# Kernel optimization log

Hardware: AMD Instinct MI355X
Metric: run time of the kernel (lower is better)

Reference implementation:

```python
import jax, jax.numpy as jnp
import numpy as np

D_MODEL = 1024
N_HEADS = 16
D_K = D_MODEL // N_HEADS


def setup_inputs() -> dict:
    key = jax.random.key(0)
    ks = jax.random.split(key, 12)
    B, S, D, H = 2, 2048, D_MODEL, N_HEADS
    s = 1.0 / np.sqrt(D)
    inp = {
        "x": jax.random.normal(ks[0], (B, S, D), jnp.float32),
        "Wq": jax.random.normal(ks[1], (D, D), jnp.float32) * s,
        "bq": jnp.zeros((D,), jnp.float32),
        "Wk": jax.random.normal(ks[2], (D, D), jnp.float32) * s,
        "bk": jnp.zeros((D,), jnp.float32),
        "Wv": jax.random.normal(ks[3], (D, D), jnp.float32) * s,
        "bv": jnp.zeros((D,), jnp.float32),
        "Wo": jax.random.normal(ks[4], (D, D), jnp.float32) * s,
        "bo": jnp.zeros((D,), jnp.float32),
        "Wp": jax.random.normal(ks[5], (D, H), jnp.float32) * s,
        "bp": jnp.zeros((H,), jnp.float32),
        "alpha": jax.random.normal(ks[6], (H,), jnp.float32) * 0.1,
    }
    return inp


def reference(x, Wq, bq, Wk, bk, Wv, bv, Wo, bo, Wp, bp, alpha):
    B, S, D = x.shape
    H, dk = N_HEADS, D_K
    scale = dk ** -0.5
    # projections -> (B, H, S, dk)
    Q = (x @ Wq + bq).reshape(B, S, H, dk).transpose(0, 2, 1, 3)
    K = (x @ Wk + bk).reshape(B, S, H, dk).transpose(0, 2, 1, 3)
    V = (x @ Wv + bv).reshape(B, S, H, dk).transpose(0, 2, 1, 3)
    scores = jnp.einsum("bhid,bhjd->bhij", Q, K) * scale  # (B,H,S,S)
    # phase derived from x: (B,S,H) -> (B,H,S)
    phase = (x @ Wp + bp).transpose(0, 2, 1)
    # coherence(i,j) = cos(phi_i - phi_j), per batch/head
    coherence = jnp.cos(phase[:, :, :, None] - phase[:, :, None, :])
    scores = scores + alpha[None, :, None, None] * coherence
    attn = jax.nn.softmax(scores, axis=-1)
    out = jnp.einsum("bhij,bhjd->bhid", attn, V)  # (B,H,S,dk)
    out = out.transpose(0, 2, 1, 3).reshape(B, S, D)
    return out @ Wo + bo
```

## Files before the change

### kernel.cpp

```cpp
#include <hip/hip_runtime.h>
#include <math.h>


#define S_LEN 2048
#define NHEADS 16

typedef __attribute__((ext_vector_type(8))) short short8;
typedef __attribute__((ext_vector_type(4))) float floatx4;
typedef __attribute__((ext_vector_type(4))) unsigned int uintx4;

__device__ inline unsigned short f2bf(float f) {
    union { float f; unsigned int i; } v; v.f = f;
    unsigned int u = v.i;
    return (unsigned short)((u + 0x7fffu + ((u >> 16) & 1u)) >> 16);
}
__device__ inline unsigned int pack2_bf16(float hi, float lo) {
    union { float f; unsigned int u; } a, b; a.f = hi; b.f = lo;
    return __builtin_amdgcn_perm(a.u, b.u, 0x07060302u);
}
__device__ inline void async_copy16(const unsigned short* src, unsigned short* dst_lds) {
    __builtin_amdgcn_global_load_lds(
        (const __attribute__((address_space(1))) unsigned int*)(src),
        (__attribute__((address_space(3))) unsigned int*)(dst_lds), 16, 0, 0);
}
__device__ inline void async_copy4(const float* src, float* dst_lds) {
    __builtin_amdgcn_global_load_lds(
        (const __attribute__((address_space(1))) unsigned int*)(src),
        (__attribute__((address_space(3))) unsigned int*)(dst_lds), 4, 0, 0);
}

__global__ __launch_bounds__(256) void prep_kernel(
    const float* __restrict__ x, const float* __restrict__ Wp,
    const float* __restrict__ bp,
    const float* __restrict__ w0, const float* __restrict__ w1,
    const float* __restrict__ w2, const float* __restrict__ w3,
    unsigned short* __restrict__ d0, unsigned short* __restrict__ d1,
    unsigned short* __restrict__ d2, unsigned short* __restrict__ d3,
    float* __restrict__ cosP, float* __restrict__ sinP,
    unsigned short* __restrict__ xb) {
    __shared__ __align__(16) unsigned short shmem[64 * 72];
    int t = threadIdx.x;
    if (blockIdx.x < 4096) {
        float* red = reinterpret_cast<float*>(shmem);
        int bid = blockIdx.x;
        int b = bid >> 11, s = bid & 2047;
        int h = t & 15, c = t >> 4;
        const float* xr = x + (size_t)bid * 1024;
        {
            float4 xv = *reinterpret_cast<const float4*>(&xr[t * 4]);
            uint2 o;
            o.x = (unsigned int)f2bf(xv.x) | ((unsigned int)f2bf(xv.y) << 16);
            o.y = (unsigned int)f2bf(xv.z) | ((unsigned int)f2bf(xv.w) << 16);
            *reinterpret_cast<uint2*>(&xb[(size_t)bid * 1024 + t * 4]) = o;
        }
        float acc = 0.f;
#pragma unroll 8
        for (int kk = 0; kk < 64; kk++) {
            int k = c * 64 + kk;
            acc += xr[k] * Wp[k * 16 + h];
        }
        red[t] = acc;
        __syncthreads();
        if (t < 16) {
            float sum = 0.f;
#pragma unroll
            for (int c2 = 0; c2 < 16; c2++) sum += red[c2 * 16 + t];
            sum += bp[t];
            float sv, cv;
            __sincosf(sum, &sv, &cv);
            size_t o = ((size_t)b * NHEADS + t) * S_LEN + s;
            cosP[o] = cv; sinP[o] = sv;
        }
    } else {
        unsigned short (*tile)[72] = reinterpret_cast<unsigned short (*)[72]>(shmem);
        int bid = blockIdx.x - 4096;
        int mat = bid >> 8;
        int tl  = bid & 255;
        int tr = tl >> 4, tc = tl & 15;
        const float* src    = (mat == 0) ? w0 : (mat == 1) ? w1 : (mat == 2) ? w2 : w3;
        unsigned short* dst = (mat == 0) ? d0 : (mat == 1) ? d1 : (mat == 2) ? d2 : d3;
        int col = t & 63, rbase = (t >> 6) * 16;
#pragma unroll
        for (int i = 0; i < 16; i++) {
            int row = rbase + i;
            tile[row][col] = f2bf(src[(size_t)(tr * 64 + row) * 1024 + tc * 64 + col]);
        }
        __syncthreads();
#pragma unroll
        for (int i = 0; i < 16; i++) {
            int row = rbase + i;
            dst[(size_t)(tc * 64 + row) * 1024 + tr * 64 + col] = tile[col][row];
        }
    }
}

template <int MT>
__global__ __launch_bounds__(256) void gemm_bt(
    const unsigned short* __restrict__ A, const unsigned short* __restrict__ BT,
    int N, int mode,
    const float* __restrict__ b0, const float* __restrict__ b1,
    const float* __restrict__ b2,
    unsigned short* __restrict__ o0, unsigned short* __restrict__ o1,
    unsigned short* __restrict__ o2, float* __restrict__ of) {
    __shared__ __align__(16) unsigned short As[MT * 32];
    __shared__ __align__(16) unsigned short Bs[128 * 32];
    const int K = 1024;
    const int MI = MT / 32;
    int t = threadIdx.x;
    int mBase = blockIdx.x * MT;
    int nBase = blockIdx.y * 128;
    int w = t >> 6, lane = t & 63, l15 = lane & 15, quad = lane >> 4;
    int wm = (w & 1) * (MT / 2), wn = (w >> 1) * 64;
    floatx4 acc[MI][4];
#pragma unroll
    for (int i = 0; i < MI; i++)
#pragma unroll
        for (int j = 0; j < 4; j++) acc[i][j] = (floatx4){0.f, 0.f, 0.f, 0.f};

    int arow = t >> 2, aseg = (t & 3) * 8;
    for (int k0 = 0; k0 < K; k0 += 32) {
        __syncthreads();
#pragma unroll
        for (int i = 0; i < MT / 64; i++)
            async_copy16(&A[(size_t)(mBase + i * 64 + arow) * K + k0 + aseg],
                         &As[(i * 64 + arow) * 32 + aseg]);
#pragma unroll
        for (int i = 0; i < 2; i++)
            async_copy16(&BT[(size_t)(nBase + i * 64 + arow) * K + k0 + aseg],
                         &Bs[(i * 64 + arow) * 32 + aseg]);
        __syncthreads();
        short8 af[MI], bfr[4];
#pragma unroll
        for (int mi = 0; mi < MI; mi++)
            af[mi] = *reinterpret_cast<const short8*>(&As[(wm + mi * 16 + l15) * 32 + quad * 8]);
#pragma unroll
        for (int ni = 0; ni < 4; ni++)
            bfr[ni] = *reinterpret_cast<const short8*>(&Bs[(wn + ni * 16 + l15) * 32 + quad * 8]);
#pragma unroll
        for (int mi = 0; mi < MI; mi++)
#pragma unroll
            for (int ni = 0; ni < 4; ni++)
                acc[mi][ni] = __builtin_amdgcn_mfma_f32_16x16x32_bf16(af[mi], bfr[ni], acc[mi][ni], 0, 0, 0);
    }

#pragma unroll
    for (int mi = 0; mi < MI; mi++) {
        int rowB = mBase + wm + mi * 16 + quad * 4;
#pragma unroll
        for (int ni = 0; ni < 4; ni++) {
            int col = nBase + wn + ni * 16 + l15;
            if (mode == 0) {
                float bias = b0[col];
#pragma unroll
                for (int r = 0; r < 4; r++) {
                    of[(size_t)(rowB + r) * N + col] = acc[mi][ni][r] + bias;
                }
            } else {
                int mat = col >> 10, nn = col & 1023;
                int h = nn >> 6, d = nn & 63;
                int b = rowB >> 11, sidx = rowB & 2047;
                if (mat == 2) {
                    float bv = b2[nn];
                    int jj = sidx & 63;
                    int a2 = jj >> 5, c2 = (jj >> 4) & 1, bb = jj & 15;
                    size_t rowOff = ((size_t)((b * NHEADS + h) * 64 + d)) * S_LEN +
                                    (sidx & ~63) + a2 * 32 + c2;
#pragma unroll
                    for (int r = 0; r < 4; r++)
                        o2[rowOff + 2 * (bb + r)] = f2bf(acc[mi][ni][r] + bv);
                } else {
                    const float* bias  = (mat == 0) ? b0 : b1;
                    unsigned short* op = (mat == 0) ? o0 : o1;
                    float bv = bias[nn];
                    float scl = (mat == 0) ? 0.18033688f : 1.0f;
#pragma unroll
                    for (int r = 0; r < 4; r++) {
                        float cv = (acc[mi][ni][r] + bv) * scl;
                        op[(((size_t)b * NHEADS + h) * S_LEN + (sidx + r)) * 64 + d] = f2bf(cv);
                    }
                }
            }
        }
    }
}

__global__ __launch_bounds__(512) void attn_kernel(
    const unsigned short* __restrict__ Qg, const unsigned short* __restrict__ Kg,
    const unsigned short* __restrict__ VTg,
    const float* __restrict__ cosP, const float* __restrict__ sinP,
    const float* __restrict__ alpha, unsigned short* __restrict__ ctx) {
    __shared__ __align__(16) unsigned short KsB[2][64 * 64];
    __shared__ __align__(16) unsigned short VtB[2][64 * 64];
    __shared__ __align__(16) float csB[2][128];
    __shared__ __align__(16) unsigned short Plb[8][16 * 72];

    int bid = blockIdx.x;
    int bh = bid >> 4, qt = bid & 15;
    int t = threadIdx.x, w = t >> 6, lane = t & 63, l15 = lane & 15, quad = lane >> 4;
    int m0 = qt * 128 + w * 16;
    size_t base = (size_t)bh * (S_LEN * 64);
    size_t phBase = (size_t)bh * S_LEN;
    const float L2E = 1.44269504f;

    int sj = t >> 3, sg = t & 7;
    int srot = ((sg - (sj & 7)) & 7) * 8;

    short8 qf[2];
#pragma unroll
    for (int c = 0; c < 2; c++)
        qf[c] = *reinterpret_cast<const short8*>(
            &Qg[base + (size_t)(m0 + l15) * 64 + c * 32 + quad * 8]);

    float alph = alpha[bh & 15] * L2E;
    float ci[4], si[4];
#pragma unroll
    for (int r = 0; r < 4; r++) {
        size_t o = phBase + m0 + quad * 4 + r;
        ci[r] = alph * cosP[o];
        si[r] = alph * sinP[o];
    }

    {
        async_copy16(&Kg[base + (size_t)sj * 64 + srot], &KsB[0][t * 8]);
        async_copy16(&VTg[base + (size_t)sj * S_LEN + srot], &VtB[0][t * 8]);
        if (w == 2)      async_copy4(&cosP[phBase + lane], &csB[0][lane]);
        else if (w == 3) async_copy4(&sinP[phBase + lane], &csB[0][64 + lane]);
    }

    floatx4 oacc[4], lacc;
#pragma unroll
    for (int tt = 0; tt < 4; tt++) oacc[tt] = (floatx4){0.f, 0.f, 0.f, 0.f};
    lacc = (floatx4){0.f, 0.f, 0.f, 0.f};
    const short8 ones8 = {(short)0x3F80, (short)0x3F80, (short)0x3F80, (short)0x3F80,
                          (short)0x3F80, (short)0x3F80, (short)0x3F80, (short)0x3F80};

    int rot = l15 & 7;
    int cb0 = 16 * ((quad + rot) & 7);
    int cb1 = 16 * ((quad + 4 + rot) & 7);

    for (int kt = 0; kt < 32; kt++) {
        int p = kt & 1;
        __syncthreads();
        if (kt < 31) {
            int kn = kt + 1, pn = p ^ 1;
            async_copy16(&Kg[base + (size_t)(kn * 64 + sj) * 64 + srot], &KsB[pn][t * 8]);
            async_copy16(&VTg[base + (size_t)sj * S_LEN + kn * 64 + srot], &VtB[pn][t * 8]);
            if (w == 2)      async_copy4(&cosP[phBase + kn * 64 + lane], &csB[pn][lane]);
            else if (w == 3) async_copy4(&sinP[phBase + kn * 64 + lane], &csB[pn][64 + lane]);
        }

        floatx4 st[4];
#pragma unroll
        for (int jt = 0; jt < 4; jt++) {
            const char* kr = (const char*)&KsB[p][(jt * 16 + l15) * 64];
            short8 kf0 = *reinterpret_cast<const short8*>(kr + cb0);
            short8 kf1 = *reinterpret_cast<const short8*>(kr + cb1);
            floatx4 s = (floatx4){0.f, 0.f, 0.f, 0.f};
            s = __builtin_amdgcn_mfma_f32_16x16x32_bf16(qf[0], kf0, s, 0, 0, 0);
            s = __builtin_amdgcn_mfma_f32_16x16x32_bf16(qf[1], kf1, s, 0, 0, 0);
            st[jt] = s;
        }

        float cjv[4], sjv[4];
#pragma unroll
        for (int jt = 0; jt < 4; jt++) {
            cjv[jt] = csB[p][jt * 16 + l15];
            sjv[jt] = csB[p][64 + jt * 16 + l15];
        }

        unsigned int* pl = reinterpret_cast<unsigned int*>(&Plb[w][0]);
#pragma unroll
        for (int r = 0; r < 4; r++) {
            float cc = ci[r], ss = si[r];
            float p0 = __builtin_amdgcn_exp2f(st[0][r] + cc * cjv[0] + ss * sjv[0]);
            float p1 = __builtin_amdgcn_exp2f(st[1][r] + cc * cjv[1] + ss * sjv[1]);
            float p2 = __builtin_amdgcn_exp2f(st[2][r] + cc * cjv[2] + ss * sjv[2]);
            float p3 = __builtin_amdgcn_exp2f(st[3][r] + cc * cjv[3] + ss * sjv[3]);
            int row = quad * 4 + r;
            pl[row * 36 + l15]      = pack2_bf16(p1, p0);
            pl[row * 36 + 16 + l15] = pack2_bf16(p3, p2);
        }

        short8 pf[2];
#pragma unroll
        for (int c = 0; c < 2; c++)
            pf[c] = *reinterpret_cast<const short8*>(
                &Plb[w][l15 * 72 + c * 32 + quad * 8]);

#pragma unroll
        for (int c = 0; c < 2; c++) {
            int cb = c ? cb1 : cb0;
#pragma unroll
            for (int tt = 0; tt < 4; tt++) {
                const char* vr = (const char*)&VtB[p][(tt * 16 + l15) * 64];
                short8 vf = *reinterpret_cast<const short8*>(vr + cb);
                oacc[tt] = __builtin_amdgcn_mfma_f32_16x16x32_bf16(pf[c], vf, oacc[tt], 0, 0, 0);
            }
            lacc = __builtin_amdgcn_mfma_f32_16x16x32_bf16(pf[c], ones8, lacc, 0, 0, 0);
        }
    }

    int b = bh >> 4, h = bh & 15;
    float inv[4];
#pragma unroll
    for (int r = 0; r < 4; r++) inv[r] = 1.0f / lacc[r];
#pragma unroll
    for (int tt = 0; tt < 4; tt++)
#pragma unroll
        for (int r = 0; r < 4; r++) {
            int srow = m0 + quad * 4 + r;
            ctx[((size_t)(b * S_LEN + srow)) * 1024 + h * 64 + tt * 16 + l15] =
                f2bf(oacc[tt][r] * inv[r]);
        }
}

extern "C" void kernel_launch(void* const* d_in, const int* in_sizes, int n_in,
                              void* d_out, int out_size, void* d_ws, size_t ws_size,
                              hipStream_t stream) {
    const float* x     = (const float*)d_in[0];
    const float* Wq    = (const float*)d_in[1];
    const float* bq    = (const float*)d_in[2];
    const float* Wk    = (const float*)d_in[3];
    const float* bk    = (const float*)d_in[4];
    const float* Wv    = (const float*)d_in[5];
    const float* bv    = (const float*)d_in[6];
    const float* Wo    = (const float*)d_in[7];
    const float* bo    = (const float*)d_in[8];
    const float* Wp    = (const float*)d_in[9];
    const float* bp    = (const float*)d_in[10];
    const float* alpha = (const float*)d_in[11];
    float* out = (float*)d_out;

    const size_t MB = 1048576;
    char* ws = (char*)d_ws;
    unsigned short* WT   = (unsigned short*)(ws);
    unsigned short* WoT  = (unsigned short*)(ws + 6 * MB);
    unsigned short* xb   = (unsigned short*)(ws + 8 * MB);
    unsigned short* ctx  = (unsigned short*)(ws + 8 * MB);
    unsigned short* Qw   = (unsigned short*)(ws + 16 * MB);
    unsigned short* Kw   = (unsigned short*)(ws + 24 * MB);
    unsigned short* VTg  = (unsigned short*)(ws + 32 * MB);
    float* cosP          = (float*)(ws + 40 * MB);
    float* sinP          = (float*)(ws + 40 * MB + 262144);

    prep_kernel<<<dim3(5120), dim3(256), 0, stream>>>(
        x, Wp, bp, Wq, Wk, Wv, Wo,
        WT, WT + 1048576, WT + 2097152, WoT, cosP, sinP, xb);
    gemm_bt<128><<<dim3(32, 24), dim3(256), 0, stream>>>(
        xb, WT, 3072, 1, bq, bk, bv, Qw, Kw, VTg, (float*)nullptr);
    attn_kernel<<<dim3(512), dim3(512), 0, stream>>>(
        Qw, Kw, VTg, cosP, sinP, alpha, ctx);
    gemm_bt<64><<<dim3(64, 8), dim3(256), 0, stream>>>(
        ctx, WoT, 1024, 0, bo, bo, bo,
        (unsigned short*)nullptr, (unsigned short*)nullptr,
        (unsigned short*)nullptr, out);
}
```

Before: 221.2 us.

## Fold phase coherence into QK matmul and switch attention to 32x32 MFMA

Uses cos(a-b)=cos a cos b + sin a sin b to fold the alpha-scaled coherence term into an extra MFMA K-slice. Q gets an augmented [alpha*cos, alpha*sin, 0...] vector and K gets [cos, sin, 0...], both stored as padded bf16 by the prep kernel. The attention kernel moves from 16x16x32 to 32x32x16 MFMA with 4 waves of 32 query rows each. P now stays in registers as the B-operand layout instead of going through an LDS round trip, and the V-transpose store is repacked into vectorized writes. This removes per-element coherence FMAs and the P shared-memory traffic, at the cost of bf16 precision on the phase terms and an extra padded MFMA per tile.

```diff
diff --git a/kernel.cpp b/kernel.cpp
--- a/kernel.cpp
+++ b/kernel.cpp
@@ -7,7 +7,7 @@
 
 typedef __attribute__((ext_vector_type(8))) short short8;
 typedef __attribute__((ext_vector_type(4))) float floatx4;
-typedef __attribute__((ext_vector_type(4))) unsigned int uintx4;
+typedef __attribute__((ext_vector_type(16))) float floatx16;
 
 __device__ inline unsigned short f2bf(float f) {
     union { float f; unsigned int i; } v; v.f = f;
@@ -23,20 +23,21 @@
         (const __attribute__((address_space(1))) unsigned int*)(src),
         (__attribute__((address_space(3))) unsigned int*)(dst_lds), 16, 0, 0);
 }
-__device__ inline void async_copy4(const float* src, float* dst_lds) {
-    __builtin_amdgcn_global_load_lds(
-        (const __attribute__((address_space(1))) unsigned int*)(src),
-        (__attribute__((address_space(3))) unsigned int*)(dst_lds), 4, 0, 0);
+__device__ inline floatx16 zero16() {
+    floatx16 v;
+#pragma unroll
+    for (int i = 0; i < 16; i++) v[i] = 0.f;
+    return v;
 }
 
 __global__ __launch_bounds__(256) void prep_kernel(
     const float* __restrict__ x, const float* __restrict__ Wp,
-    const float* __restrict__ bp,
+    const float* __restrict__ bp, const float* __restrict__ alpha,
     const float* __restrict__ w0, const float* __restrict__ w1,
     const float* __restrict__ w2, const float* __restrict__ w3,
     unsigned short* __restrict__ d0, unsigned short* __restrict__ d1,
     unsigned short* __restrict__ d2, unsigned short* __restrict__ d3,
-    float* __restrict__ cosP, float* __restrict__ sinP,
+    unsigned short* __restrict__ qcs, unsigned short* __restrict__ kcs,
     unsigned short* __restrict__ xb) {
     __shared__ __align__(16) unsigned short shmem[64 * 72];
     int t = threadIdx.x;
@@ -68,8 +69,17 @@
             sum += bp[t];
             float sv, cv;
             __sincosf(sum, &sv, &cv);
-            size_t o = ((size_t)b * NHEADS + t) * S_LEN + s;
-            cosP[o] = cv; sinP[o] = sv;
+            float as = alpha[t] * 1.44269504f;
+            size_t off = ((size_t)(b * NHEADS + t) * S_LEN + s) * 16;
+            uint4 qv = make_uint4(
+                (unsigned int)f2bf(as * cv) | ((unsigned int)f2bf(as * sv) << 16), 0u, 0u, 0u);
+            uint4 kv = make_uint4(
+                (unsigned int)f2bf(cv) | ((unsigned int)f2bf(sv) << 16), 0u, 0u, 0u);
+            uint4 z = make_uint4(0u, 0u, 0u, 0u);
+            *reinterpret_cast<uint4*>(&qcs[off]) = qv;
+            *reinterpret_cast<uint4*>(&qcs[off + 8]) = z;
+            *reinterpret_cast<uint4*>(&kcs[off]) = kv;
+            *reinterpret_cast<uint4*>(&kcs[off + 8]) = z;
         }
     } else {
         unsigned short (*tile)[72] = reinterpret_cast<unsigned short (*)[72]>(shmem);
@@ -161,13 +171,15 @@
                 int b = rowB >> 11, sidx = rowB & 2047;
                 if (mat == 2) {
                     float bv = b2[nn];
-                    int jj = sidx & 63;
-                    int a2 = jj >> 5, c2 = (jj >> 4) & 1, bb = jj & 15;
+                    unsigned int lo = (unsigned int)f2bf(acc[mi][ni][0] + bv) |
+                                      ((unsigned int)f2bf(acc[mi][ni][1] + bv) << 16);
+                    unsigned int hi = (unsigned int)f2bf(acc[mi][ni][2] + bv) |
+                                      ((unsigned int)f2bf(acc[mi][ni][3] + bv) << 16);
+                    int jj = sidx & 15;
+                    int s23 = ((jj & 4) << 1) | ((jj & 8) >> 1);
                     size_t rowOff = ((size_t)((b * NHEADS + h) * 64 + d)) * S_LEN +
-                                    (sidx & ~63) + a2 * 32 + c2;
-#pragma unroll
-                    for (int r = 0; r < 4; r++)
-                        o2[rowOff + 2 * (bb + r)] = f2bf(acc[mi][ni][r] + bv);
+                                    (sidx & ~15) + s23;
+                    *reinterpret_cast<uint2*>(&o2[rowOff]) = make_uint2(lo, hi);
                 } else {
                     const float* bias  = (mat == 0) ? b0 : b1;
                     unsigned short* op = (mat == 0) ? o0 : o1;
@@ -184,134 +196,117 @@
     }
 }
 
-__global__ __launch_bounds__(512) void attn_kernel(
-    const unsigned short* __restrict__ Qg, const unsigned short* __restrict__ Kg,
-    const unsigned short* __restrict__ VTg,
-    const float* __restrict__ cosP, const float* __restrict__ sinP,
-    const float* __restrict__ alpha, unsigned short* __restrict__ ctx) {
-    __shared__ __align__(16) unsigned short KsB[2][64 * 64];
-    __shared__ __align__(16) unsigned short VtB[2][64 * 64];
-    __shared__ __align__(16) float csB[2][128];
-    __shared__ __align__(16) unsigned short Plb[8][16 * 72];
+__global__ __launch_bounds__(256) void attn_kernel(
+    const unsigned short* __restrict__ Qg, const unsigned short* __restrict__ Qcs,
+    const unsigned short* __restrict__ Kg, const unsigned short* __restrict__ Kcs,
+    const unsigned short* __restrict__ VTg, unsigned short* __restrict__ ctx) {
+    __shared__ __align__(16) unsigned short KdB[2][4096];
+    __shared__ __align__(16) unsigned short KcB[2][1024];
+    __shared__ __align__(16) unsigned short VtB[2][4096];
 
     int bid = blockIdx.x;
     int bh = bid >> 4, qt = bid & 15;
-    int t = threadIdx.x, w = t >> 6, lane = t & 63, l15 = lane & 15, quad = lane >> 4;
-    int m0 = qt * 128 + w * 16;
+    int t = threadIdx.x, lane = t & 63, w = t >> 6;
+    int l31 = lane & 31, g = lane >> 5;
+    int i0w = qt * 128 + w * 32;
     size_t base = (size_t)bh * (S_LEN * 64);
-    size_t phBase = (size_t)bh * S_LEN;
-    const float L2E = 1.44269504f;
-
-    int sj = t >> 3, sg = t & 7;
-    int srot = ((sg - (sj & 7)) & 7) * 8;
-
-    short8 qf[2];
-#pragma unroll
-    for (int c = 0; c < 2; c++)
-        qf[c] = *reinterpret_cast<const short8*>(
-            &Qg[base + (size_t)(m0 + l15) * 64 + c * 32 + quad * 8]);
-
-    float alph = alpha[bh & 15] * L2E;
-    float ci[4], si[4];
-#pragma unroll
-    for (int r = 0; r < 4; r++) {
-        size_t o = phBase + m0 + quad * 4 + r;
-        ci[r] = alph * cosP[o];
-        si[r] = alph * sinP[o];
-    }
-
+    size_t basec = (size_t)bh * (S_LEN * 16);
+
+    short8 qd[4], qc;
     {
-        async_copy16(&Kg[base + (size_t)sj * 64 + srot], &KsB[0][t * 8]);
-        async_copy16(&VTg[base + (size_t)sj * S_LEN + srot], &VtB[0][t * 8]);
-        if (w == 2)      async_copy4(&cosP[phBase + lane], &csB[0][lane]);
-        else if (w == 3) async_copy4(&sinP[phBase + lane], &csB[0][64 + lane]);
-    }
-
-    floatx4 oacc[4], lacc;
-#pragma unroll
-    for (int tt = 0; tt < 4; tt++) oacc[tt] = (floatx4){0.f, 0.f, 0.f, 0.f};
-    lacc = (floatx4){0.f, 0.f, 0.f, 0.f};
+        const unsigned short* qrow = Qg + base + (size_t)(i0w + l31) * 64;
+#pragma unroll
+        for (int f = 0; f < 4; f++)
+            qd[f] = *reinterpret_cast<const short8*>(qrow + f * 16 + g * 8);
+        qc = *reinterpret_cast<const short8*>(Qcs + basec + (size_t)(i0w + l31) * 16 + g * 8);
+    }
+
+    int srow = t >> 3;
+    int scol = (((t & 7) - ((srow >> 2) & 7)) & 7) * 8;
+    const unsigned short* kd0 = Kg + base + (size_t)srow * 64 + scol;
+    const unsigned short* kd1 = Kg + base + (size_t)(srow + 32) * 64 + scol;
+    const unsigned short* vv0 = VTg + base + (size_t)srow * S_LEN + scol;
+    const unsigned short* vv1 = VTg + base + (size_t)(srow + 32) * S_LEN + scol;
+    const unsigned short* kcc = Kcs + basec + t * 8;
+
+    async_copy16(kd0, &KdB[0][t * 8]);
+    async_copy16(kd1, &KdB[0][2048 + t * 8]);
+    async_copy16(vv0, &VtB[0][t * 8]);
+    async_copy16(vv1, &VtB[0][2048 + t * 8]);
+    if (t < 128) async_copy16(kcc, &KcB[0][t * 8]);
+
+    floatx16 o0 = zero16(), o1 = zero16(), lac = zero16();
     const short8 ones8 = {(short)0x3F80, (short)0x3F80, (short)0x3F80, (short)0x3F80,
                           (short)0x3F80, (short)0x3F80, (short)0x3F80, (short)0x3F80};
 
-    int rot = l15 & 7;
-    int cb0 = 16 * ((quad + rot) & 7);
-    int cb1 = 16 * ((quad + 4 + rot) & 7);
+    int rot = (l31 >> 2) & 7;
+    int fo[4];
+#pragma unroll
+    for (int f = 0; f < 4; f++) fo[f] = ((2 * f + g + rot) & 7) * 8;
+    int arow = l31 * 64;
+    int kcof = l31 * 16 + g * 8;
 
     for (int kt = 0; kt < 32; kt++) {
         int p = kt & 1;
         __syncthreads();
         if (kt < 31) {
             int kn = kt + 1, pn = p ^ 1;
-            async_copy16(&Kg[base + (size_t)(kn * 64 + sj) * 64 + srot], &KsB[pn][t * 8]);
-            async_copy16(&VTg[base + (size_t)sj * S_LEN + kn * 64 + srot], &VtB[pn][t * 8]);
-            if (w == 2)      async_copy4(&cosP[phBase + kn * 64 + lane], &csB[pn][lane]);
-            else if (w == 3) async_copy4(&sinP[phBase + kn * 64 + lane], &csB[pn][64 + lane]);
-        }
-
-        floatx4 st[4];
-#pragma unroll
-        for (int jt = 0; jt < 4; jt++) {
-            const char* kr = (const char*)&KsB[p][(jt * 16 + l15) * 64];
-            short8 kf0 = *reinterpret_cast<const short8*>(kr + cb0);
-            short8 kf1 = *reinterpret_cast<const short8*>(kr + cb1);
-            floatx4 s = (floatx4){0.f, 0.f, 0.f, 0.f};
-            s = __builtin_amdgcn_mfma_f32_16x16x32_bf16(qf[0], kf0, s, 0, 0, 0);
-            s = __builtin_amdgcn_mfma_f32_16x16x32_bf16(qf[1], kf1, s, 0, 0, 0);
-            st[jt] = s;
-        }
-
-        float cjv[4], sjv[4];
-#pragma unroll
-        for (int jt = 0; jt < 4; jt++) {
-            cjv[jt] = csB[p][jt * 16 + l15];
-            sjv[jt] = csB[p][64 + jt * 16 + l15];
-        }
-
-        unsigned int* pl = reinterpret_cast<unsigned int*>(&Plb[w][0]);
-#pragma unroll
-        for (int r = 0; r < 4; r++) {
-            float cc = ci[r], ss = si[r];
-            float p0 = __builtin_amdgcn_exp2f(st[0][r] + cc * cjv[0] + ss * sjv[0]);
-            float p1 = __builtin_amdgcn_exp2f(st[1][r] + cc * cjv[1] + ss * sjv[1]);
-            float p2 = __builtin_amdgcn_exp2f(st[2][r] + cc * cjv[2] + ss * sjv[2]);
-            float p3 = __builtin_amdgcn_exp2f(st[3][r] + cc * cjv[3] + ss * sjv[3]);
-            int row = quad * 4 + r;
-            pl[row * 36 + l15]      = pack2_bf16(p1, p0);
-            pl[row * 36 + 16 + l15] = pack2_bf16(p3, p2);
-        }
-
-        short8 pf[2];
-#pragma unroll
-        for (int c = 0; c < 2; c++)
-            pf[c] = *reinterpret_cast<const short8*>(
-                &Plb[w][l15 * 72 + c * 32 + quad * 8]);
-
-#pragma unroll
-        for (int c = 0; c < 2; c++) {
-            int cb = c ? cb1 : cb0;
-#pragma unroll
-            for (int tt = 0; tt < 4; tt++) {
-                const char* vr = (const char*)&VtB[p][(tt * 16 + l15) * 64];
-                short8 vf = *reinterpret_cast<const short8*>(vr + cb);
-                oacc[tt] = __builtin_amdgcn_mfma_f32_16x16x32_bf16(pf[c], vf, oacc[tt], 0, 0, 0);
+            async_copy16(kd0 + kn * 4096, &KdB[pn][t * 8]);
+            async_copy16(kd1 + kn * 4096, &KdB[pn][2048 + t * 8]);
+            async_copy16(vv0 + kn * 64, &VtB[pn][t * 8]);
+            async_copy16(vv1 + kn * 64, &VtB[pn][2048 + t * 8]);
+            if (t < 128) async_copy16(kcc + kn * 1024, &KcB[pn][t * 8]);
+        }
+
+        short8 pf[4];
+#pragma unroll
+        for (int jt = 0; jt < 2; jt++) {
+            const unsigned short* kb = &KdB[p][jt * 2048 + arow];
+            floatx16 st = zero16();
+            st = __builtin_amdgcn_mfma_f32_32x32x16_bf16(
+                *reinterpret_cast<const short8*>(kb + fo[0]), qd[0], st, 0, 0, 0);
+            st = __builtin_amdgcn_mfma_f32_32x32x16_bf16(
+                *reinterpret_cast<const short8*>(kb + fo[1]), qd[1], st, 0, 0, 0);
+            st = __builtin_amdgcn_mfma_f32_32x32x16_bf16(
+                *reinterpret_cast<const short8*>(kb + fo[2]), qd[2], st, 0, 0, 0);
+            st = __builtin_amdgcn_mfma_f32_32x32x16_bf16(
+                *reinterpret_cast<const short8*>(kb + fo[3]), qd[3], st, 0, 0, 0);
+            st = __builtin_amdgcn_mfma_f32_32x32x16_bf16(
+                *reinterpret_cast<const short8*>(&KcB[p][jt * 512 + kcof]), qc, st, 0, 0, 0);
+            float pe[16];
+#pragma unroll
+            for (int r = 0; r < 16; r++) pe[r] = __builtin_amdgcn_exp2f(st[r]);
+#pragma unroll
+            for (int h = 0; h < 2; h++) {
+                union { unsigned int u[4]; short8 s; } pk;
+                pk.u[0] = pack2_bf16(pe[8 * h + 1], pe[8 * h + 0]);
+                pk.u[1] = pack2_bf16(pe[8 * h + 3], pe[8 * h + 2]);
+                pk.u[2] = pack2_bf16(pe[8 * h + 5], pe[8 * h + 4]);
+                pk.u[3] = pack2_bf16(pe[8 * h + 7], pe[8 * h + 6]);
+                pf[2 * jt + h] = pk.s;
             }
-            lacc = __builtin_amdgcn_mfma_f32_16x16x32_bf16(pf[c], ones8, lacc, 0, 0, 0);
+        }
+
+#pragma unroll
+        for (int c = 0; c < 4; c++) {
+            lac = __builtin_amdgcn_mfma_f32_32x32x16_bf16(pf[c], ones8, lac, 0, 0, 0);
+            int vo = ((2 * c + g + rot) & 7) * 8;
+            short8 vf0 = *reinterpret_cast<const short8*>(&VtB[p][arow + vo]);
+            short8 vf1 = *reinterpret_cast<const short8*>(&VtB[p][2048 + arow + vo]);
+            o0 = __builtin_amdgcn_mfma_f32_32x32x16_bf16(pf[c], vf0, o0, 0, 0, 0);
+            o1 = __builtin_amdgcn_mfma_f32_32x32x16_bf16(pf[c], vf1, o1, 0, 0, 0);
         }
     }
 
     int b = bh >> 4, h = bh & 15;
-    float inv[4];
-#pragma unroll
-    for (int r = 0; r < 4; r++) inv[r] = 1.0f / lacc[r];
-#pragma unroll
-    for (int tt = 0; tt < 4; tt++)
-#pragma unroll
-        for (int r = 0; r < 4; r++) {
-            int srow = m0 + quad * 4 + r;
-            ctx[((size_t)(b * S_LEN + srow)) * 1024 + h * 64 + tt * 16 + l15] =
-                f2bf(oacc[tt][r] * inv[r]);
-        }
+#pragma unroll
+    for (int r = 0; r < 16; r++) {
+        int i = i0w + (r & 3) + 8 * (r >> 2) + 4 * g;
+        float inv = 1.0f / lac[r];
+        size_t off = ((size_t)(b * S_LEN + i)) * 1024 + h * 64;
+        ctx[off + l31]      = f2bf(o0[r] * inv);
+        ctx[off + 32 + l31] = f2bf(o1[r] * inv);
+    }
 }
 
 extern "C" void kernel_launch(void* const* d_in, const int* in_sizes, int n_in,
@@ -340,16 +335,16 @@
     unsigned short* Qw   = (unsigned short*)(ws + 16 * MB);
     unsigned short* Kw   = (unsigned short*)(ws + 24 * MB);
     unsigned short* VTg  = (unsigned short*)(ws + 32 * MB);
-    float* cosP          = (float*)(ws + 40 * MB);
-    float* sinP          = (float*)(ws + 40 * MB + 262144);
+    unsigned short* Qcs  = (unsigned short*)(ws + 40 * MB);
+    unsigned short* Kcs  = (unsigned short*)(ws + 42 * MB);
 
     prep_kernel<<<dim3(5120), dim3(256), 0, stream>>>(
-        x, Wp, bp, Wq, Wk, Wv, Wo,
-        WT, WT + 1048576, WT + 2097152, WoT, cosP, sinP, xb);
+        x, Wp, bp, alpha, Wq, Wk, Wv, Wo,
+        WT, WT + 1048576, WT + 2097152, WoT, Qcs, Kcs, xb);
     gemm_bt<128><<<dim3(32, 24), dim3(256), 0, stream>>>(
         xb, WT, 3072, 1, bq, bk, bv, Qw, Kw, VTg, (float*)nullptr);
-    attn_kernel<<<dim3(512), dim3(512), 0, stream>>>(
-        Qw, Kw, VTg, cosP, sinP, alpha, ctx);
+    attn_kernel<<<dim3(512), dim3(256), 0, stream>>>(
+        Qw, Qcs, Kw, Kcs, VTg, ctx);
     gemm_bt<64><<<dim3(64, 8), dim3(256), 0, stream>>>(
         ctx, WoT, 1024, 0, bo, bo, bo,
         (unsigned short*)nullptr, (unsigned short*)nullptr,
```

Measured after the change: 230.9 us. 4.4% more time.
